# Kernel optimization log

Measured on AMD Instinct MI355X. Metric: run time of the kernel, lower is better.

Reference implementation:

```python
import jax, jax.numpy as jnp
import numpy as np

N = 50000      # nodes
E = 800000     # adjacency edges (A support)
EM = 2000000   # masked observed pairs (M support)
EL = 200000    # link-prediction label edges
FEAT, EMB, HID, OUT, STEPS = 128, 8, 128, 64, 5


def setup_inputs() -> dict:
    key = jax.random.key(0)
    ks = jax.random.split(key, 12)
    x_feat = jax.random.normal(ks[0], (N, FEAT), jnp.float32)
    x_init = 0.1 * jax.random.normal(ks[1], (N, EMB), jnp.float32)
    edge_index = jax.random.randint(ks[2], (2, E), 0, N)
    edge_index_2 = jax.random.randint(ks[3], (2, EM), 0, N)
    mask_edges = edge_index_2  # mask.nonzero().t() -> same observed-pair support
    edge_label_index = jax.random.randint(ks[4], (2, EL), 0, N)
    # Q is the diag(+-1) indefinite-metric matrix of gLASE
    signs = jnp.where(jax.random.bernoulli(ks[5], 0.5, (EMB,)), 1.0, -1.0)
    Q = jnp.diag(signs).astype(jnp.float32)
    # learned per-step GD step-size matrices (small init = small GD steps)
    Wgd1 = 0.01 * jax.random.normal(ks[6], (STEPS, EMB, EMB), jnp.float32)
    Wgd2 = 0.01 * jax.random.normal(ks[7], (STEPS, EMB, EMB), jnp.float32)
    # GCNConv weights (glorot-ish)
    Wc1 = jax.random.normal(ks[8], (FEAT + EMB, HID), jnp.float32) / np.sqrt(FEAT + EMB)
    bc1 = jnp.zeros((HID,), jnp.float32)
    Wc2 = jax.random.normal(ks[9], (HID, OUT), jnp.float32) / np.sqrt(HID)
    bc2 = jnp.zeros((OUT,), jnp.float32)
    return dict(x_feat=x_feat, x_init=x_init, Q=Q, Wgd1=Wgd1, Wgd2=Wgd2,
                Wc1=Wc1, bc1=bc1, Wc2=Wc2, bc2=bc2,
                edge_index=edge_index, edge_index_2=edge_index_2,
                mask_edges=mask_edges, edge_label_index=edge_label_index)


def _encode(x_feat, x_init, Q, Wgd1, Wgd2, Wc1, bc1, Wc2, bc2,
            edge_index, mask_edges):
    n = x_feat.shape[0]
    seg = lambda d, i: jax.ops.segment_sum(d, i, num_segments=n)
    src, dst = edge_index[0], edge_index[1]
    msrc, mdst = mask_edges[0], mask_edges[1]

    def gcn(x, W, b):
        # PyG GCNConv: add self-loops, symmetric deg^-1/2 normalization
        deg = seg(jnp.ones(src.shape[0], x.dtype), dst) + 1.0
        dinv = jax.lax.rsqrt(deg)
        h = x @ W
        out = seg(h[src] * (dinv[src] * dinv[dst])[:, None], dst)
        return out + h * (dinv * dinv)[:, None] + b

    # GD_Block unroll: X <- X + (M.A) X W1 Q  -  (M.(X Q X^T)) X W2 Q
    x = x_init
    for t in range(Wgd1.shape[0]):
        t1 = seg(((x @ Wgd1[t]) @ Q)[src], dst)                     # (M.A) X W1 Q
        w = jnp.sum((x @ Q)[msrc] * x[mdst], axis=-1)               # (X Q X^T) on M support
        t2 = seg(w[:, None] * ((x @ Wgd2[t]) @ Q)[mdst], msrc)      # masked quadratic term
        x = x + t1 - t2
    x_emb = x

    h = jax.nn.relu(gcn(jnp.concatenate([x_feat, x_emb], axis=1), Wc1, bc1))
    z = gcn(h, Wc2, bc2)
    return z, x_emb


def reference(x_feat, x_init, Q, Wgd1, Wgd2, Wc1, bc1, Wc2, bc2,
              edge_index, edge_index_2, mask_edges, edge_label_index):
    z, x_emb = _encode(x_feat, x_init, Q, Wgd1, Wgd2, Wc1, bc1, Wc2, bc2,
                       edge_index, mask_edges)
    # decode: dot-product link scores on label edges
    logits = jnp.sum(z[edge_label_index[0]] * z[edge_label_index[1]], axis=-1)
    return logits, z, x_emb
```

## Files before the change

### kernel.cpp

```cpp
#include <hip/hip_runtime.h>
#include <hip/hip_bf16.h>

typedef __hip_bfloat16 bf16;
typedef unsigned short u16;
typedef __attribute__((ext_vector_type(8))) short bf16x8;
typedef __attribute__((ext_vector_type(4))) short short4v;
typedef __attribute__((ext_vector_type(4))) float f32x4;

#define CAPA 64
#define CAPM 96
#define GSTR 16
#define NBMAX 512
#define SORTT 8192

__device__ __forceinline__ float b2f(bf16 v){ return __bfloat162float(v); }
__device__ __forceinline__ bf16  f2b(float v){ return __float2bfloat16(v); }
__device__ __forceinline__ short f2bs(float v){ union{ bf16 b; short s; } u; u.b = f2b(v); return u.s; }
__device__ __forceinline__ float uf(unsigned u){ return __uint_as_float(u); }
__device__ __forceinline__ void unpack8(uint4 u, float* f){
  f[0]=uf(u.x<<16); f[1]=uf(u.x&0xFFFF0000u);
  f[2]=uf(u.y<<16); f[3]=uf(u.y&0xFFFF0000u);
  f[4]=uf(u.z<<16); f[5]=uf(u.z&0xFFFF0000u);
  f[6]=uf(u.w<<16); f[7]=uf(u.w&0xFFFF0000u);
}
__device__ __forceinline__ float dinv_of(int endv, int node, int cap){
  return __frsqrt_rn((float)(endv - node*cap) + 1.0f);
}

__global__ void k_sniff_init(const unsigned* __restrict__ q, int* __restrict__ flag,
                             int* __restrict__ gcnt, int n){
  int i = blockIdx.x*blockDim.x + threadIdx.x;
  if (i == 0){
    unsigned u = q[0];
    *flag = (u == 0x3F800000u || u == 0xBF800000u) ? 0 : 1;
  }
  if (i < 2*NBMAX*GSTR) gcnt[i] = 0;
  (void)n;
}

__global__ void k_prep(const void* __restrict__ Q, const void* __restrict__ W1,
                       const void* __restrict__ W2, const void* __restrict__ b1,
                       const void* __restrict__ b2,
                       const void* __restrict__ Wc1, const void* __restrict__ Wc2,
                       float* __restrict__ qf, float* __restrict__ w1,
                       float* __restrict__ w2, float* __restrict__ bb1,
                       float* __restrict__ bb2,
                       bf16* __restrict__ wsw1, bf16* __restrict__ wsw2,
                       int steps, const int* __restrict__ flag){
  int isbf = *flag;
  int tid = threadIdx.x;
  #define CV(p,i) (isbf ? b2f(((const bf16*)(p))[i]) : ((const float*)(p))[i])
  if (blockIdx.x == 0){
    if (tid < 64)  qf[tid]  = CV(Q, tid);
    if (tid < 128) bb1[tid] = CV(b1, tid);
    if (tid < 64)  bb2[tid] = CV(b2, tid);
    for (int i = tid; i < steps*64; i += blockDim.x){
      w1[i] = CV(W1, i);
      w2[i] = CV(W2, i);
    }
  } else if (blockIdx.x <= 80){
    int t = (blockIdx.x-1)*256 + tid;
    if (t < 8*5*512){
      int j = t & 7, lane = (t >> 3) & 63, rest = t >> 9;
      int kb = rest % 5, ct = rest / 5;
      int k = kb*32 + (lane>>4)*8 + j;
      int nn = ct*16 + (lane&15);
      float v = (k < 136) ? CV(Wc1, (size_t)k*128+nn) : 0.f;
      wsw1[t] = f2b(v);
    }
  } else {
    int t = (blockIdx.x-81)*256 + tid;
    if (t < 4*4*512){
      int j = t & 7, lane = (t >> 3) & 63, rest = t >> 9;
      int kb = rest & 3, ct = rest >> 2;
      int k = kb*32 + (lane>>4)*8 + j;
      int nn = ct*16 + (lane&15);
      float v = CV(Wc2, (size_t)k*64+nn);
      wsw2[t] = f2b(v);
    }
  }
  #undef CV
}

__global__ void k_sort(const int* __restrict__ key, const int* __restrict__ val,
                       int ne, unsigned* __restrict__ stage, int capB,
                       int* __restrict__ gcnt, int nb){
  __shared__ int hist[NBMAX];
  __shared__ int base[NBMAX];
  int tid = threadIdx.x;
  for (int i = tid; i < nb; i += 256) hist[i] = 0;
  __syncthreads();
  int t0 = blockIdx.x * SORTT;
  unsigned pk[32];
  #pragma unroll
  for (int j = 0; j < 32; j++){
    int e = t0 + j*256 + tid;
    if (e < ne){
      unsigned k = (unsigned)key[e], v = (unsigned)val[e];
      pk[j] = (k << 16) | (v & 0xFFFFu);
      atomicAdd(&hist[k >> 7], 1);
    } else pk[j] = 0xFFFFFFFFu;
  }
  __syncthreads();
  for (int i = tid; i < nb; i += 256){
    int c = hist[i];
    base[i] = c ? atomicAdd(&gcnt[(size_t)i*GSTR], c) : 0;
    hist[i] = 0;
  }
  __syncthreads();
  #pragma unroll
  for (int j = 0; j < 32; j++){
    if (pk[j] != 0xFFFFFFFFu){
      int b = (int)(pk[j] >> 23);
      int r = atomicAdd(&hist[b], 1);
      int idx = base[b] + r;
      if (idx < capB) stage[(size_t)b*capB + idx] = pk[j];
    }
  }
}

__global__ void k_scat2(const unsigned* __restrict__ stage, int capB,
                        const int* __restrict__ gcnt, u16* __restrict__ col,
                        int* __restrict__ endX, int cap, int n){
  __shared__ int cur[128];
  int tid = threadIdx.x;
  int b = blockIdx.x;
  if (tid < 128) cur[tid] = 0;
  __syncthreads();
  int cnt = gcnt[(size_t)b*GSTR]; if (cnt > capB) cnt = capB;
  const unsigned* sr = stage + (size_t)b*capB;
  for (int i = tid; i < cnt; i += 256){
    unsigned pk = sr[i];
    int k = (int)(pk >> 16);
    int pos = atomicAdd(&cur[k & 127], 1);
    if (pos < cap) col[(size_t)k*cap + pos] = (u16)(pk & 0xFFFFu);
  }
  __syncthreads();
  if (tid < 128){
    int node = (b << 7) + tid;
    if (node < n){
      int c = cur[tid]; if (c > cap) c = cap;
      endX[node] = node*cap + c;
    }
  }
}

__global__ void k_gd_pre0(const void* __restrict__ xraw, const int* __restrict__ flag,
                          const float* __restrict__ qf_g,
                          const float* __restrict__ W1, const float* __restrict__ W2,
                          float* __restrict__ xa, float* __restrict__ xq,
                          bf16* __restrict__ y1b, bf16* __restrict__ xy2b, int n){
  __shared__ float qf[64], w1q[64], w2q[64];
  int tid = threadIdx.x;
  if (tid < 64) qf[tid] = qf_g[tid];
  __syncthreads();
  if (tid < 64){
    int k = tid >> 3, j = tid & 7;
    float a1 = 0.f, a2 = 0.f;
    #pragma unroll
    for (int m = 0; m < 8; m++){
      a1 += W1[k*8+m] * qf[m*8+j];
      a2 += W2[k*8+m] * qf[m*8+j];
    }
    w1q[tid] = a1; w2q[tid] = a2;
  }
  __syncthreads();
  int node = blockIdx.x*blockDim.x + tid;
  if (node >= n) return;
  int isbf = *flag;
  float xv[8], o1[8], o2[8], oq[8];
  #pragma unroll
  for (int j = 0; j < 8; j++){
    xv[j] = isbf ? b2f(((const bf16*)xraw)[(size_t)node*8+j])
                 : ((const float*)xraw)[(size_t)node*8+j];
    o1[j]=o2[j]=oq[j]=0.f;
  }
  #pragma unroll
  for (int k = 0; k < 8; k++){
    #pragma unroll
    for (int j = 0; j < 8; j++){
      o1[j] += xv[k]*w1q[k*8+j];
      o2[j] += xv[k]*w2q[k*8+j];
      oq[j] += xv[k]*qf[k*8+j];
    }
  }
  #pragma unroll
  for (int j = 0; j < 8; j++){
    xa[(size_t)node*8+j] = xv[j];
    xq[(size_t)node*8+j] = oq[j];
  }
  short4v p0, p1;
  #pragma unroll
  for (int j = 0; j < 4; j++){ p0[j] = f2bs(o1[j]); p1[j] = f2bs(o1[j+4]); }
  *(short4v*)(y1b + (size_t)node*8)     = p0;
  *(short4v*)(y1b + (size_t)node*8 + 4) = p1;
  short4v q0, q1, q2, q3;
  #pragma unroll
  for (int j = 0; j < 4; j++){
    q0[j] = f2bs(xv[j]);   q1[j] = f2bs(xv[j+4]);
    q2[j] = f2bs(o2[j]);   q3[j] = f2bs(o2[j+4]);
  }
  bf16* r = xy2b + (size_t)node*16;
  *(short4v*)(r)    = q0; *(short4v*)(r+4)  = q1;
  *(short4v*)(r+8)  = q2; *(short4v*)(r+12) = q3;
}

__global__ void k_gd_step(const float* __restrict__ x, const float* __restrict__ xq_r,
                          const bf16* __restrict__ y1b_r, const bf16* __restrict__ xy2b_r,
                          const int* __restrict__ endA, const u16* __restrict__ colA,
                          const int* __restrict__ endM, const u16* __restrict__ colM,
                          float* __restrict__ xout, int n,
                          void* __restrict__ outbase, int elemoff,
                          const int* __restrict__ flag, int do_out, int do_pre,
                          const float* __restrict__ qf_g,
                          const float* __restrict__ W1n, const float* __restrict__ W2n,
                          float* __restrict__ xq_w, bf16* __restrict__ y1b_w,
                          bf16* __restrict__ xy2b_w){
  __shared__ float qfs[64], w1qs[64], w2qs[64];
  if (do_pre){
    int tid = threadIdx.x;
    if (tid < 64) qfs[tid] = qf_g[tid];
    __syncthreads();
    if (tid < 64){
      int k = tid >> 3, j = tid & 7;
      float a1 = 0.f, a2 = 0.f;
      #pragma unroll
      for (int m = 0; m < 8; m++){
        a1 += W1n[k*8+m] * qfs[m*8+j];
        a2 += W2n[k*8+m] * qfs[m*8+j];
      }
      w1qs[tid] = a1; w2qs[tid] = a2;
    }
    __syncthreads();
  }

  int node = blockIdx.x*(blockDim.x>>4) + (threadIdx.x>>4);
  if (node >= n) return;
  int lane = threadIdx.x & 15;
  float acc[8];
  #pragma unroll
  for (int j = 0; j < 8; j++) acc[j] = 0.f;

  {
    int s = node*CAPA, e = endA[node];
    int i = s + lane;
    while (i < e){
      int i2 = i + 16;
      int s0 = colA[i];
      int s1 = (i2 < e) ? colA[i2] : s0;
      uint4 u0 = *(const uint4*)(y1b_r + (size_t)s0*8);
      uint4 u1 = *(const uint4*)(y1b_r + (size_t)s1*8);
      float f[8];
      unpack8(u0, f);
      #pragma unroll
      for (int j = 0; j < 8; j++) acc[j] += f[j];
      if (i2 < e){
        unpack8(u1, f);
        #pragma unroll
        for (int j = 0; j < 8; j++) acc[j] += f[j];
      }
      i += 32;
    }
  }

  {
    float q[8];
    #pragma unroll
    for (int j = 0; j < 8; j++) q[j] = xq_r[(size_t)node*8+j];
    int s = node*CAPM, e = endM[node];
    int i = s + lane;
    while (i < e){
      int i2 = i + 16;
      int m0 = colM[i];
      int m1 = (i2 < e) ? colM[i2] : m0;
      const uint4* r0 = (const uint4*)(xy2b_r + (size_t)m0*16);
      const uint4* r1 = (const uint4*)(xy2b_r + (size_t)m1*16);
      uint4 a0 = r0[0], b0 = r0[1];
      uint4 a1 = r1[0], b1 = r1[1];
      float xm[8], y2[8];
      unpack8(a0, xm); unpack8(b0, y2);
      float w = q[0]*xm[0]+q[1]*xm[1]+q[2]*xm[2]+q[3]*xm[3]
              + q[4]*xm[4]+q[5]*xm[5]+q[6]*xm[6]+q[7]*xm[7];
      #pragma unroll
      for (int j = 0; j < 8; j++) acc[j] -= w*y2[j];
      if (i2 < e){
        unpack8(a1, xm); unpack8(b1, y2);
        w = q[0]*xm[0]+q[1]*xm[1]+q[2]*xm[2]+q[3]*xm[3]
          + q[4]*xm[4]+q[5]*xm[5]+q[6]*xm[6]+q[7]*xm[7];
        #pragma unroll
        for (int j = 0; j < 8; j++) acc[j] -= w*y2[j];
      }
      i += 32;
    }
  }

  #pragma unroll
  for (int j = 0; j < 8; j++){
    #pragma unroll
    for (int off = 8; off; off >>= 1) acc[j] += __shfl_xor(acc[j], off, 16);
  }

  float xo[8];
  #pragma unroll
  for (int j = 0; j < 8; j++) xo[j] = x[(size_t)node*8+j] + acc[j];

  if (lane == 0){
    #pragma unroll
    for (int j = 0; j < 8; j++) xout[(size_t)node*8+j] = xo[j];
    if (do_out){
      if (*flag){
        bf16* ob = (bf16*)outbase + elemoff + (size_t)node*8;
        #pragma unroll
        for (int j = 0; j < 8; j++) ob[j] = f2b(xo[j]);
      } else {
        float* of = (float*)outbase + elemoff + (size_t)node*8;
        #pragma unroll
        for (int j = 0; j < 8; j++) of[j] = xo[j];
      }
    }
  }

  if (do_pre){
    if (lane < 8){
      int j = lane;
      float v1 = 0.f, v2 = 0.f;
      #pragma unroll
      for (int k = 0; k < 8; k++){
        v1 += xo[k]*qfs[k*8+j];
        v2 += xo[k]*w2qs[k*8+j];
      }
      xq_w[(size_t)node*8+j] = v1;
      xy2b_w[(size_t)node*16+8+j] = f2b(v2);
    } else {
      int j = lane - 8;
      float v1 = 0.f;
      #pragma unroll
      for (int k = 0; k < 8; k++) v1 += xo[k]*w1qs[k*8+j];
      y1b_w[(size_t)node*8+j] = f2b(v1);
      xy2b_w[(size_t)node*16+j] = f2b(xo[j]);
    }
  }
}

__global__ void k_mm1_mfma(const void* __restrict__ xfeat, const float* __restrict__ xemb,
                           const bf16* __restrict__ Wsw, const int* __restrict__ endA,
                           bf16* __restrict__ h, const int* __restrict__ flag, int n){
  int lane = threadIdx.x & 63;
  int wv = threadIdx.x >> 6;
  int node = blockIdx.x*64 + wv*16 + (lane & 15);
  int quad = lane >> 4;
  int nodec = node < n ? node : (n-1);
  int isbf = *flag;

  bf16x8 xb[5];
  if (isbf){
    const bf16* xr = (const bf16*)xfeat + (size_t)nodec*128;
    #pragma unroll
    for (int kb = 0; kb < 4; kb++)
      xb[kb] = *(const bf16x8*)(xr + kb*32 + quad*8);
  } else {
    const float* xr = (const float*)xfeat + (size_t)nodec*128;
    #pragma unroll
    for (int kb = 0; kb < 4; kb++){
      const float* pp = xr + kb*32 + quad*8;
      bf16x8 t;
      #pragma unroll
      for (int j = 0; j < 8; j++) t[j] = f2bs(pp[j]);
      xb[kb] = t;
    }
  }
  {
    bf16x8 t;
    if (quad == 0){
      const float* ep = xemb + (size_t)nodec*8;
      #pragma unroll
      for (int j = 0; j < 8; j++) t[j] = f2bs(ep[j]);
    } else {
      #pragma unroll
      for (int j = 0; j < 8; j++) t[j] = 0;
    }
    xb[4] = t;
  }

  f32x4 acc[8];
  #pragma unroll
  for (int ct = 0; ct < 8; ct++) acc[ct] = (f32x4){0.f,0.f,0.f,0.f};

  #pragma unroll
  for (int kb = 0; kb < 5; kb++){
    #pragma unroll
    for (int ct = 0; ct < 8; ct++){
      bf16x8 wa = *(const bf16x8*)(Wsw + ((size_t)(ct*5 + kb)*64 + lane)*8);
      acc[ct] = __builtin_amdgcn_mfma_f32_16x16x32_bf16(wa, xb[kb], acc[ct], 0, 0, 0);
    }
  }

  if (node >= n) return;
  float dn = dinv_of(endA[node], node, CAPA);
  bf16* hr = h + (size_t)node*128;
  #pragma unroll
  for (int ct = 0; ct < 8; ct++){
    short4v pk;
    #pragma unroll
    for (int r = 0; r < 4; r++) pk[r] = f2bs(acc[ct][r] * dn);
    *(short4v*)(hr + ct*16 + quad*4) = pk;
  }
}

__global__ void k_mm2_mfma(const bf16* __restrict__ h1, const bf16* __restrict__ Wsw,
                           const int* __restrict__ endA, float* __restrict__ h2, int n){
  int lane = threadIdx.x & 63;
  int wv = threadIdx.x >> 6;
  int node = blockIdx.x*64 + wv*16 + (lane & 15);
  int quad = lane >> 4;
  int nodec = node < n ? node : (n-1);

  const bf16* xr = h1 + (size_t)nodec*128;
  bf16x8 xb[4];
  #pragma unroll
  for (int kb = 0; kb < 4; kb++)
    xb[kb] = *(const bf16x8*)(xr + kb*32 + quad*8);

  f32x4 acc[4];
  #pragma unroll
  for (int ct = 0; ct < 4; ct++) acc[ct] = (f32x4){0.f,0.f,0.f,0.f};

  #pragma unroll
  for (int kb = 0; kb < 4; kb++){
    #pragma unroll
    for (int ct = 0; ct < 4; ct++){
      bf16x8 wa = *(const bf16x8*)(Wsw + ((size_t)(ct*4 + kb)*64 + lane)*8);
      acc[ct] = __builtin_amdgcn_mfma_f32_16x16x32_bf16(wa, xb[kb], acc[ct], 0, 0, 0);
    }
  }

  if (node >= n) return;
  float dn = dinv_of(endA[node], node, CAPA);
  float* hr = h2 + (size_t)node*64;
  #pragma unroll
  for (int ct = 0; ct < 4; ct++){
    f32x4 o;
    #pragma unroll
    for (int r = 0; r < 4; r++) o[r] = acc[ct][r] * dn;
    *(f32x4*)(hr + ct*16 + quad*4) = o;
  }
}

__global__ void k_agg1(const bf16* __restrict__ h, const float* __restrict__ bias,
                       const int* __restrict__ endA, const u16* __restrict__ col,
                       bf16* __restrict__ out, int n, int gper){
  int pass = blockIdx.x / gper;
  int node = (blockIdx.x % gper)*(blockDim.x>>4) + (threadIdx.x>>4);
  if (node >= n) return;
  int choff = 32*pass;
  int lane = threadIdx.x & 15;
  int bu = (choff>>1) + lane;
  unsigned uself = ((const unsigned*)(h + (size_t)node*128))[bu];
  float p0[4], p1[4];
  p0[0] = uf(uself << 16); p1[0] = uf(uself & 0xFFFF0000u);
  p0[1]=p0[2]=p0[3]=0.f; p1[1]=p1[2]=p1[3]=0.f;
  int s = node*CAPA, e = endA[node];
  for (int base = s; base < e; base += 16){
    int cnt = e - base; if (cnt > 16) cnt = 16;
    int cv = col[base + (lane < cnt ? lane : 0)];
    int j = 0;
    for (; j + 4 <= cnt; j += 4){
      int s0 = __shfl(cv, j,   16);
      int s1 = __shfl(cv, j+1, 16);
      int s2 = __shfl(cv, j+2, 16);
      int s3 = __shfl(cv, j+3, 16);
      unsigned u0 = ((const unsigned*)(h + (size_t)s0*128))[bu];
      unsigned u1 = ((const unsigned*)(h + (size_t)s1*128))[bu];
      unsigned u2 = ((const unsigned*)(h + (size_t)s2*128))[bu];
      unsigned u3 = ((const unsigned*)(h + (size_t)s3*128))[bu];
      p0[0] += uf(u0 << 16); p1[0] += uf(u0 & 0xFFFF0000u);
      p0[1] += uf(u1 << 16); p1[1] += uf(u1 & 0xFFFF0000u);
      p0[2] += uf(u2 << 16); p1[2] += uf(u2 & 0xFFFF0000u);
      p0[3] += uf(u3 << 16); p1[3] += uf(u3 & 0xFFFF0000u);
    }
    for (; j < cnt; j++){
      int s0 = __shfl(cv, j, 16);
      unsigned u0 = ((const unsigned*)(h + (size_t)s0*128))[bu];
      p0[0] += uf(u0 << 16); p1[0] += uf(u0 & 0xFFFF0000u);
    }
  }
  float dn = dinv_of(e, node, CAPA);
  int ch = choff + 2*lane;
  float f0 = (p0[0]+p0[1]+p0[2]+p0[3])*dn + bias[ch];
  float f1 = (p1[0]+p1[1]+p1[2]+p1[3])*dn + bias[ch+1];
  f0 = fmaxf(f0, 0.f); f1 = fmaxf(f1, 0.f);
  union { unsigned u; bf16 b[2]; } pk;
  pk.b[0] = f2b(f0); pk.b[1] = f2b(f1);
  ((unsigned*)(out + (size_t)node*128))[bu] = pk.u;
}

__global__ void k_agg2(const float* __restrict__ h, const float* __restrict__ bias,
                       const int* __restrict__ endA, const u16* __restrict__ col,
                       bf16* __restrict__ zbf, void* __restrict__ outbase, int elemoff,
                       const int* __restrict__ flag, int n, int gper){
  int pass = blockIdx.x / gper;
  int node = (blockIdx.x % gper)*(blockDim.x>>4) + (threadIdx.x>>4);
  if (node >= n) return;
  int lane = threadIdx.x & 15;
  int ch = 16*pass + lane;
  float a[4];
  a[0] = h[(size_t)node*64 + ch];
  a[1]=a[2]=a[3]=0.f;
  int s = node*CAPA, e = endA[node];
  for (int base = s; base < e; base += 16){
    int cnt = e - base; if (cnt > 16) cnt = 16;
    int cv = col[base + (lane < cnt ? lane : 0)];
    int j = 0;
    for (; j + 4 <= cnt; j += 4){
      int s0 = __shfl(cv, j,   16);
      int s1 = __shfl(cv, j+1, 16);
      int s2 = __shfl(cv, j+2, 16);
      int s3 = __shfl(cv, j+3, 16);
      a[0] += h[(size_t)s0*64 + ch];
      a[1] += h[(size_t)s1*64 + ch];
      a[2] += h[(size_t)s2*64 + ch];
      a[3] += h[(size_t)s3*64 + ch];
    }
    for (; j < cnt; j++){
      int s0 = __shfl(cv, j, 16);
      a[0] += h[(size_t)s0*64 + ch];
    }
  }
  float f = (a[0]+a[1]+a[2]+a[3])*dinv_of(e, node, CAPA) + bias[ch];
  size_t idx = (size_t)node*64 + ch;
  zbf[idx] = f2b(f);
  if (*flag) ((bf16*)outbase)[elemoff + idx] = f2b(f);
  else       ((float*)outbase)[elemoff + idx] = f;
}

__global__ void k_decode(const bf16* __restrict__ zbf, const int* __restrict__ eli,
                         void* __restrict__ outbase, const int* __restrict__ flag, int ne){
  int e = blockIdx.x*(blockDim.x>>5) + (threadIdx.x>>5);
  if (e >= ne) return;
  int lane = threadIdx.x & 31;
  int a = eli[e], b = eli[ne + e];
  unsigned ua = ((const unsigned*)zbf)[(size_t)a*32 + lane];
  unsigned ub = ((const unsigned*)zbf)[(size_t)b*32 + lane];
  float p = uf(ua<<16)*uf(ub<<16) + uf(ua&0xFFFF0000u)*uf(ub&0xFFFF0000u);
  #pragma unroll
  for (int off = 16; off; off >>= 1) p += __shfl_xor(p, off, 32);
  if (lane == 0){
    if (*flag) ((bf16*)outbase)[e] = f2b(p);
    else       ((float*)outbase)[e] = p;
  }
}

extern "C" void kernel_launch(void* const* d_in, const int* in_sizes, int n_in,
                              void* d_out, int out_size, void* d_ws, size_t ws_size,
                              hipStream_t stream){
  const void* x_feat = d_in[0];
  const void* x_init = d_in[1];
  const void* Q      = d_in[2];
  const void* Wgd1   = d_in[3];
  const void* Wgd2   = d_in[4];
  const void* Wc1    = d_in[5];
  const void* bc1    = d_in[6];
  const void* Wc2    = d_in[7];
  const void* bc2    = d_in[8];
  const int*  ei     = (const int*)d_in[9];
  const int*  me     = (const int*)d_in[11];
  const int*  eli    = (const int*)d_in[12];

  const int N     = in_sizes[1] / 8;
  const int E     = in_sizes[9] / 2;
  const int EM    = in_sizes[11] / 2;
  const int EL    = in_sizes[12] / 2;
  const int STEPS = in_sizes[3] / 64;

  char* p = (char*)d_ws;
  auto alloc = [&](size_t bytes)->char*{
    char* r = p; p += (bytes + 255) & ~(size_t)255; return r;
  };
  float* x_a   = (float*)alloc((size_t)N*8*4);
  float* x_b   = (float*)alloc((size_t)N*8*4);
  float* xqA   = (float*)alloc((size_t)N*8*4);
  float* xqB   = (float*)alloc((size_t)N*8*4);
  bf16*  y1bA  = (bf16*)alloc((size_t)N*8*2);
  bf16*  y1bB  = (bf16*)alloc((size_t)N*8*2);
  bf16*  xy2bA = (bf16*)alloc((size_t)N*16*2);
  bf16*  xy2bB = (bf16*)alloc((size_t)N*16*2);
  int*   curA  = (int*)alloc((size_t)N*4);
  int*   curM  = (int*)alloc((size_t)N*4);
  u16*   colA  = (u16*)alloc((size_t)N*CAPA*2);
  u16*   colM  = (u16*)alloc((size_t)N*CAPM*2);
  float* qf_s  = (float*)alloc(64*4);
  float* wg1_s = (float*)alloc((size_t)STEPS*64*4);
  float* wg2_s = (float*)alloc((size_t)STEPS*64*4);
  bf16*  wsw1  = (bf16*)alloc((size_t)8*5*512*2);
  bf16*  wsw2  = (bf16*)alloc((size_t)4*4*512*2);
  float* bc1_s = (float*)alloc(128*4);
  float* bc2_s = (float*)alloc(64*4);
  int*   flag  = (int*)alloc(4);
  int*   gcnt  = (int*)alloc((size_t)2*NBMAX*GSTR*4);
  bf16*  zbf   = (bf16*)alloc((size_t)N*64*2);
  char*  bufA  = alloc((size_t)N*128*2);
  char*  bufB  = alloc((size_t)N*128*2);

  bf16*  h  = (bf16*)bufA;
  bf16*  h1 = (bf16*)bufB;
  float* h2 = (float*)bufA;

  unsigned* stM = (unsigned*)bufA;
  unsigned* stA = (unsigned*)bufB;
  int* gcntA = gcnt;
  int* gcntM = gcnt + NBMAX*GSTR;

  int nb = (N + 127) >> 7;
  int capBA = E/nb + E/(nb*4) + 256;
  int capBM = EM/nb + EM/(nb*4) + 256;
  int cA = (int)(((size_t)N*64) / (size_t)nb);
  if (capBA > cA) capBA = cA;
  if (capBM > cA) capBM = cA;

  const int* src  = ei;
  const int* dst  = ei + E;
  const int* msrc = me;

  float* xqS[2]   = {xqA, xqB};
  bf16*  y1bS[2]  = {y1bA, y1bB};
  bf16*  xy2bS[2] = {xy2bA, xy2bB};

  k_sniff_init<<<(N+255)/256, 256, 0, stream>>>((const unsigned*)Q, flag, gcnt, N);
  k_prep<<<113, 256, 0, stream>>>(Q, Wgd1, Wgd2, bc1, bc2, Wc1, Wc2,
                                  qf_s, wg1_s, wg2_s, bc1_s, bc2_s,
                                  wsw1, wsw2, STEPS, flag);

  int gsA = (E + SORTT - 1) / SORTT;
  int gsM = (EM + SORTT - 1) / SORTT;
  k_sort<<<gsA, 256, 0, stream>>>(dst, src, E, stA, capBA, gcntA, nb);
  k_sort<<<gsM, 256, 0, stream>>>(msrc, me + EM, EM, stM, capBM, gcntM, nb);
  k_scat2<<<nb, 256, 0, stream>>>(stA, capBA, gcntA, colA, curA, CAPA, N);
  k_scat2<<<nb, 256, 0, stream>>>(stM, capBM, gcntM, colM, curM, CAPM, N);

  k_gd_pre0<<<(N+255)/256, 256, 0, stream>>>(x_init, flag, qf_s, wg1_s, wg2_s,
                                             x_a, xqA, y1bA, xy2bA, N);
  float* xc = x_a;
  float* xn = x_b;
  int rb = 0;
  for (int t = 0; t < STEPS; t++){
    int last = (t == STEPS-1);
    int tn = last ? (STEPS-1) : (t+1);
    k_gd_step<<<(N+15)/16, 256, 0, stream>>>(xc, xqS[rb], y1bS[rb], xy2bS[rb],
                                             curA, colA, curM, colM, xn, N,
                                             d_out, EL + N*64, flag, last, !last,
                                             qf_s, wg1_s + tn*64, wg2_s + tn*64,
                                             xqS[1-rb], y1bS[1-rb], xy2bS[1-rb]);
    float* tmp = xc; xc = xn; xn = tmp;
    rb ^= 1;
  }

  int g1 = (N+15)/16;
  k_mm1_mfma<<<(N+63)/64, 256, 0, stream>>>(x_feat, xc, wsw1, curA, h, flag, N);
  k_agg1<<<4*g1, 256, 0, stream>>>(h, bc1_s, curA, colA, h1, N, g1);
  k_mm2_mfma<<<(N+63)/64, 256, 0, stream>>>(h1, wsw2, curA, h2, N);
  k_agg2<<<4*g1, 256, 0, stream>>>(h2, bc2_s, curA, colA, zbf, d_out, EL, flag, N, g1);
  k_decode<<<(EL+7)/8, 256, 0, stream>>>(zbf, eli, d_out, flag, EL);
}
```

Measured before the change: 443.5 us.

## Widen GCN aggregation gathers to full rows and deepen masked-edge unroll

The two GCN aggregation kernels previously used four passes over the node set, each handling a channel slice with 4-byte gathers. They now process all channels in one pass, with each lane gathering 16-byte vectors (8 bf16 or 4 fp32), which cuts launch count and re-reading of adjacency indices and improves gather width. The GD step's masked-edge loop is unrolled from 2 to 4 neighbours per lane to keep more loads in flight, and the node's x row is loaded up front. The cost is more registers and fewer blocks, so occupancy may drop.

```diff
diff --git a/kernel.cpp b/kernel.cpp
--- a/kernel.cpp
+++ b/kernel.cpp
@@ -237,6 +237,11 @@
   int node = blockIdx.x*(blockDim.x>>4) + (threadIdx.x>>4);
   if (node >= n) return;
   int lane = threadIdx.x & 15;
+
+  float xbase[8];
+  #pragma unroll
+  for (int j = 0; j < 8; j++) xbase[j] = x[(size_t)node*8+j];
+
   float acc[8];
   #pragma unroll
   for (int j = 0; j < 8; j++) acc[j] = 0.f;
@@ -270,13 +275,19 @@
     int s = node*CAPM, e = endM[node];
     int i = s + lane;
     while (i < e){
-      int i2 = i + 16;
+      int i2 = i + 16, i3 = i + 32, i4 = i + 48;
       int m0 = colM[i];
       int m1 = (i2 < e) ? colM[i2] : m0;
+      int m2 = (i3 < e) ? colM[i3] : m0;
+      int m3 = (i4 < e) ? colM[i4] : m0;
       const uint4* r0 = (const uint4*)(xy2b_r + (size_t)m0*16);
       const uint4* r1 = (const uint4*)(xy2b_r + (size_t)m1*16);
+      const uint4* r2 = (const uint4*)(xy2b_r + (size_t)m2*16);
+      const uint4* r3 = (const uint4*)(xy2b_r + (size_t)m3*16);
       uint4 a0 = r0[0], b0 = r0[1];
       uint4 a1 = r1[0], b1 = r1[1];
+      uint4 a2 = r2[0], b2 = r2[1];
+      uint4 a3 = r3[0], b3 = r3[1];
       float xm[8], y2[8];
       unpack8(a0, xm); unpack8(b0, y2);
       float w = q[0]*xm[0]+q[1]*xm[1]+q[2]*xm[2]+q[3]*xm[3]
@@ -290,7 +301,21 @@
         #pragma unroll
         for (int j = 0; j < 8; j++) acc[j] -= w*y2[j];
       }
-      i += 32;
+      if (i3 < e){
+        unpack8(a2, xm); unpack8(b2, y2);
+        w = q[0]*xm[0]+q[1]*xm[1]+q[2]*xm[2]+q[3]*xm[3]
+          + q[4]*xm[4]+q[5]*xm[5]+q[6]*xm[6]+q[7]*xm[7];
+        #pragma unroll
+        for (int j = 0; j < 8; j++) acc[j] -= w*y2[j];
+      }
+      if (i4 < e){
+        unpack8(a3, xm); unpack8(b3, y2);
+        w = q[0]*xm[0]+q[1]*xm[1]+q[2]*xm[2]+q[3]*xm[3]
+          + q[4]*xm[4]+q[5]*xm[5]+q[6]*xm[6]+q[7]*xm[7];
+        #pragma unroll
+        for (int j = 0; j < 8; j++) acc[j] -= w*y2[j];
+      }
+      i += 64;
     }
   }
 
@@ -302,7 +327,7 @@
 
   float xo[8];
   #pragma unroll
-  for (int j = 0; j < 8; j++) xo[j] = x[(size_t)node*8+j] + acc[j];
+  for (int j = 0; j < 8; j++) xo[j] = xbase[j] + acc[j];
 
   if (lane == 0){
     #pragma unroll
@@ -448,17 +473,73 @@
 
 __global__ void k_agg1(const bf16* __restrict__ h, const float* __restrict__ bias,
                        const int* __restrict__ endA, const u16* __restrict__ col,
-                       bf16* __restrict__ out, int n, int gper){
-  int pass = blockIdx.x / gper;
-  int node = (blockIdx.x % gper)*(blockDim.x>>4) + (threadIdx.x>>4);
+                       bf16* __restrict__ out, int n){
+  int node = blockIdx.x*(blockDim.x>>4) + (threadIdx.x>>4);
   if (node >= n) return;
-  int choff = 32*pass;
   int lane = threadIdx.x & 15;
-  int bu = (choff>>1) + lane;
-  unsigned uself = ((const unsigned*)(h + (size_t)node*128))[bu];
-  float p0[4], p1[4];
-  p0[0] = uf(uself << 16); p1[0] = uf(uself & 0xFFFF0000u);
-  p0[1]=p0[2]=p0[3]=0.f; p1[1]=p1[2]=p1[3]=0.f;
+  uint4 uself = ((const uint4*)(h + (size_t)node*128))[lane];
+  float pa[8], pb[8], pc[8], pd[8];
+  unpack8(uself, pa);
+  #pragma unroll
+  for (int c = 0; c < 8; c++){ pb[c]=0.f; pc[c]=0.f; pd[c]=0.f; }
+  int s = node*CAPA, e = endA[node];
+  float f[8];
+  for (int base = s; base < e; base += 16){
+    int cnt = e - base; if (cnt > 16) cnt = 16;
+    int cv = col[base + (lane < cnt ? lane : 0)];
+    int j = 0;
+    for (; j + 4 <= cnt; j += 4){
+      int s0 = __shfl(cv, j,   16);
+      int s1 = __shfl(cv, j+1, 16);
+      int s2 = __shfl(cv, j+2, 16);
+      int s3 = __shfl(cv, j+3, 16);
+      uint4 u0 = ((const uint4*)(h + (size_t)s0*128))[lane];
+      uint4 u1 = ((const uint4*)(h + (size_t)s1*128))[lane];
+      uint4 u2 = ((const uint4*)(h + (size_t)s2*128))[lane];
+      uint4 u3 = ((const uint4*)(h + (size_t)s3*128))[lane];
+      unpack8(u0, f);
+      #pragma unroll
+      for (int c = 0; c < 8; c++) pa[c] += f[c];
+      unpack8(u1, f);
+      #pragma unroll
+      for (int c = 0; c < 8; c++) pb[c] += f[c];
+      unpack8(u2, f);
+      #pragma unroll
+      for (int c = 0; c < 8; c++) pc[c] += f[c];
+      unpack8(u3, f);
+      #pragma unroll
+      for (int c = 0; c < 8; c++) pd[c] += f[c];
+    }
+    for (; j < cnt; j++){
+      int s0 = __shfl(cv, j, 16);
+      uint4 u0 = ((const uint4*)(h + (size_t)s0*128))[lane];
+      unpack8(u0, f);
+      #pragma unroll
+      for (int c = 0; c < 8; c++) pa[c] += f[c];
+    }
+  }
+  float dn = dinv_of(e, node, CAPA);
+  int ch = 8*lane;
+  union { uint4 u; bf16 b[8]; } pk;
+  #pragma unroll
+  for (int c = 0; c < 8; c++){
+    float v = (pa[c]+pb[c]+pc[c]+pd[c])*dn + bias[ch+c];
+    pk.b[c] = f2b(fmaxf(v, 0.f));
+  }
+  ((uint4*)(out + (size_t)node*128))[lane] = pk.u;
+}
+
+__global__ void k_agg2(const float* __restrict__ h, const float* __restrict__ bias,
+                       const int* __restrict__ endA, const u16* __restrict__ col,
+                       bf16* __restrict__ zbf, void* __restrict__ outbase, int elemoff,
+                       const int* __restrict__ flag, int n){
+  int node = blockIdx.x*(blockDim.x>>4) + (threadIdx.x>>4);
+  if (node >= n) return;
+  int lane = threadIdx.x & 15;
+  f32x4 vs = ((const f32x4*)(h + (size_t)node*64))[lane];
+  float pa[4], pb[4], pc[4], pd[4];
+  #pragma unroll
+  for (int c = 0; c < 4; c++){ pa[c]=vs[c]; pb[c]=0.f; pc[c]=0.f; pd[c]=0.f; }
   int s = node*CAPA, e = endA[node];
   for (int base = s; base < e; base += 16){
     int cnt = e - base; if (cnt > 16) cnt = 16;
@@ -469,68 +550,39 @@
       int s1 = __shfl(cv, j+1, 16);
       int s2 = __shfl(cv, j+2, 16);
       int s3 = __shfl(cv, j+3, 16);
-      unsigned u0 = ((const unsigned*)(h + (size_t)s0*128))[bu];
-      unsigned u1 = ((const unsigned*)(h + (size_t)s1*128))[bu];
-      unsigned u2 = ((const unsigned*)(h + (size_t)s2*128))[bu];
-      unsigned u3 = ((const unsigned*)(h + (size_t)s3*128))[bu];
-      p0[0] += uf(u0 << 16); p1[0] += uf(u0 & 0xFFFF0000u);
-      p0[1] += uf(u1 << 16); p1[1] += uf(u1 & 0xFFFF0000u);
-      p0[2] += uf(u2 << 16); p1[2] += uf(u2 & 0xFFFF0000u);
-      p0[3] += uf(u3 << 16); p1[3] += uf(u3 & 0xFFFF0000u);
+      f32x4 v0 = ((const f32x4*)(h + (size_t)s0*64))[lane];
+      f32x4 v1 = ((const f32x4*)(h + (size_t)s1*64))[lane];
+      f32x4 v2 = ((const f32x4*)(h + (size_t)s2*64))[lane];
+      f32x4 v3 = ((const f32x4*)(h + (size_t)s3*64))[lane];
+      #pragma unroll
+      for (int c = 0; c < 4; c++){
+        pa[c] += v0[c]; pb[c] += v1[c]; pc[c] += v2[c]; pd[c] += v3[c];
+      }
     }
     for (; j < cnt; j++){
       int s0 = __shfl(cv, j, 16);
-      unsigned u0 = ((const unsigned*)(h + (size_t)s0*128))[bu];
-      p0[0] += uf(u0 << 16); p1[0] += uf(u0 & 0xFFFF0000u);
+      f32x4 v0 = ((const f32x4*)(h + (size_t)s0*64))[lane];
+      #pragma unroll
+      for (int c = 0; c < 4; c++) pa[c] += v0[c];
     }
   }
   float dn = dinv_of(e, node, CAPA);
-  int ch = choff + 2*lane;
-  float f0 = (p0[0]+p0[1]+p0[2]+p0[3])*dn + bias[ch];
-  float f1 = (p1[0]+p1[1]+p1[2]+p1[3])*dn + bias[ch+1];
-  f0 = fmaxf(f0, 0.f); f1 = fmaxf(f1, 0.f);
-  union { unsigned u; bf16 b[2]; } pk;
-  pk.b[0] = f2b(f0); pk.b[1] = f2b(f1);
-  ((unsigned*)(out + (size_t)node*128))[bu] = pk.u;
-}
-
-__global__ void k_agg2(const float* __restrict__ h, const float* __restrict__ bias,
-                       const int* __restrict__ endA, const u16* __restrict__ col,
-                       bf16* __restrict__ zbf, void* __restrict__ outbase, int elemoff,
-                       const int* __restrict__ flag, int n, int gper){
-  int pass = blockIdx.x / gper;
-  int node = (blockIdx.x % gper)*(blockDim.x>>4) + (threadIdx.x>>4);
-  if (node >= n) return;
-  int lane = threadIdx.x & 15;
-  int ch = 16*pass + lane;
-  float a[4];
-  a[0] = h[(size_t)node*64 + ch];
-  a[1]=a[2]=a[3]=0.f;
-  int s = node*CAPA, e = endA[node];
-  for (int base = s; base < e; base += 16){
-    int cnt = e - base; if (cnt > 16) cnt = 16;
-    int cv = col[base + (lane < cnt ? lane : 0)];
-    int j = 0;
-    for (; j + 4 <= cnt; j += 4){
-      int s0 = __shfl(cv, j,   16);
-      int s1 = __shfl(cv, j+1, 16);
-      int s2 = __shfl(cv, j+2, 16);
-      int s3 = __shfl(cv, j+3, 16);
-      a[0] += h[(size_t)s0*64 + ch];
-      a[1] += h[(size_t)s1*64 + ch];
-      a[2] += h[(size_t)s2*64 + ch];
-      a[3] += h[(size_t)s3*64 + ch];
-    }
-    for (; j < cnt; j++){
-      int s0 = __shfl(cv, j, 16);
-      a[0] += h[(size_t)s0*64 + ch];
-    }
-  }
-  float f = (a[0]+a[1]+a[2]+a[3])*dinv_of(e, node, CAPA) + bias[ch];
-  size_t idx = (size_t)node*64 + ch;
-  zbf[idx] = f2b(f);
-  if (*flag) ((bf16*)outbase)[elemoff + idx] = f2b(f);
-  else       ((float*)outbase)[elemoff + idx] = f;
+  int ch = 4*lane;
+  float fo[4];
+  #pragma unroll
+  for (int c = 0; c < 4; c++) fo[c] = (pa[c]+pb[c]+pc[c]+pd[c])*dn + bias[ch+c];
+  union { uint2 u; bf16 b[4]; } pk;
+  #pragma unroll
+  for (int c = 0; c < 4; c++) pk.b[c] = f2b(fo[c]);
+  ((uint2*)(zbf + (size_t)node*64))[lane] = pk.u;
+  if (*flag){
+    ((uint2*)((bf16*)outbase + elemoff + (size_t)node*64))[lane] = pk.u;
+  } else {
+    f32x4 o;
+    #pragma unroll
+    for (int c = 0; c < 4; c++) o[c] = fo[c];
+    ((f32x4*)((float*)outbase + elemoff + (size_t)node*64))[lane] = o;
+  }
 }
 
 __global__ void k_decode(const bf16* __restrict__ zbf, const int* __restrict__ eli,
@@ -656,8 +708,8 @@
 
   int g1 = (N+15)/16;
   k_mm1_mfma<<<(N+63)/64, 256, 0, stream>>>(x_feat, xc, wsw1, curA, h, flag, N);
-  k_agg1<<<4*g1, 256, 0, stream>>>(h, bc1_s, curA, colA, h1, N, g1);
+  k_agg1<<<g1, 256, 0, stream>>>(h, bc1_s, curA, colA, h1, N);
   k_mm2_mfma<<<(N+63)/64, 256, 0, stream>>>(h1, wsw2, curA, h2, N);
-  k_agg2<<<4*g1, 256, 0, stream>>>(h2, bc2_s, curA, colA, zbf, d_out, EL, flag, N, g1);
+  k_agg2<<<g1, 256, 0, stream>>>(h2, bc2_s, curA, colA, zbf, d_out, EL, flag, N);
   k_decode<<<(EL+7)/8, 256, 0, stream>>>(zbf, eli, d_out, flag, EL);
 }
```

Result: faster. 421.3 us (-5.0%).
